# Kernel tuning notes

Hardware: AMD Instinct MI355X
Metric: run time of the kernel (lower is better)

## Reference

```python
import jax, jax.numpy as jnp
import numpy as np
from jax import lax

K = 16          # n_neighbors
EPS_BN = 1e-6   # torch BatchNorm2d eps in source


def _bn(x, g, be):
    # training-mode batch norm over (B, N, K) per channel, biased variance
    m = jnp.mean(x, axis=(0, 2, 3), keepdims=True)
    v = jnp.var(x, axis=(0, 2, 3), keepdims=True)
    return g[None, :, None, None] * (x - m) * lax.rsqrt(v + EPS_BN) + be[None, :, None, None]


def _smlp(x, W, b, g, be, act=None):
    # SharedMLP: 1x1 conv == channel matmul, then BN, then activation
    y = jnp.einsum('oc,bcnk->bonk', W, x) + b[None, :, None, None]
    y = _bn(y, g, be)
    return act(y) if act is not None else y


def _gather(f, nbrs):
    # f: (B, C, N), nbrs: (B, N, K) -> (B, C, N, K)
    return jax.vmap(lambda fb, nb: fb[:, nb])(f, nbrs)


def _attpool(x, Ws, W, b, g, be):
    # x: (B, C, N, K); scores: linear over C, softmax over K (dim=-2 after permute)
    s = jax.nn.softmax(jnp.einsum('oc,bcnk->bonk', Ws, x), axis=-1)
    pooled = jnp.sum(s * x, axis=-1, keepdims=True)  # (B, C, N, 1)
    return _smlp(pooled, W, b, g, be, jax.nn.relu)


def setup_inputs() -> dict:
    key = jax.random.key(0)
    ks = iter(jax.random.split(key, 40))
    B, N, n_in, n_out = 2, 8192, 64, 128
    C1 = n_out // 2

    def w(shape, s=0.05):
        return jax.random.normal(next(ks), shape, jnp.float32) * s

    inp = {
        'xyz': jax.random.normal(next(ks), (B, N, 3), jnp.float32),
        'feat_in': jax.random.normal(next(ks), (B, n_in, N, 1), jnp.float32),
        'm1_w': w((C1, n_in)), 'm1_b': jnp.zeros((C1,)), 'm1_g': jnp.ones((C1,)), 'm1_be': jnp.zeros((C1,)),
        'r1_w': w((C1, 10)), 'r1_b': jnp.zeros((C1,)), 'r1_g': jnp.ones((C1,)), 'r1_be': jnp.zeros((C1,)),
        'r2_w': w((C1, C1)), 'r2_b': jnp.zeros((C1,)), 'r2_g': jnp.ones((C1,)), 'r2_be': jnp.zeros((C1,)),
        'p1s_w': w((n_out, n_out)),
        'p1_w': w((C1, n_out)), 'p1_b': jnp.zeros((C1,)), 'p1_g': jnp.ones((C1,)), 'p1_be': jnp.zeros((C1,)),
        'p2s_w': w((n_out, n_out)),
        'p2_w': w((n_out, n_out)), 'p2_b': jnp.zeros((n_out,)), 'p2_g': jnp.ones((n_out,)), 'p2_be': jnp.zeros((n_out,)),
        'm2_w': w((2 * n_out, n_out)), 'm2_b': jnp.zeros((2 * n_out,)), 'm2_g': jnp.ones((2 * n_out,)), 'm2_be': jnp.zeros((2 * n_out,)),
        'sc_w': w((2 * n_out, n_in)), 'sc_b': jnp.zeros((2 * n_out,)), 'sc_g': jnp.ones((2 * n_out,)), 'sc_be': jnp.zeros((2 * n_out,)),
    }
    return inp


def reference(xyz, feat_in,
              m1_w, m1_b, m1_g, m1_be,
              r1_w, r1_b, r1_g, r1_be,
              r2_w, r2_b, r2_g, r2_be,
              p1s_w, p1_w, p1_b, p1_g, p1_be,
              p2s_w, p2_w, p2_b, p2_g, p2_be,
              m2_w, m2_b, m2_g, m2_be,
              sc_w, sc_b, sc_g, sc_be):
    # --- naive KNN (query == support) ---
    sq = jnp.sum(xyz * xyz, axis=-1)                       # (B, N)
    d2 = sq[:, :, None] + sq[:, None, :] - 2.0 * jnp.einsum('bnd,bmd->bnm', xyz, xyz)
    neg_d2, nbrs = lax.top_k(-d2, K)                       # (B, N, K)
    dist = jnp.sqrt(jnp.maximum(-neg_d2, 1e-12))

    # --- relative position encoding (10 channels) ---
    xyz_t = jnp.swapaxes(xyz, 1, 2)                        # (B, 3, N)
    nbr_xyz = _gather(xyz_t, nbrs)                         # (B, 3, N, K)
    ctr = jnp.broadcast_to(xyz_t[..., None], nbr_xyz.shape)
    rpe = jnp.concatenate([ctr, nbr_xyz, ctr - nbr_xyz, dist[:, None]], axis=1)  # (B,10,N,K)

    rpe1 = _smlp(rpe, r1_w, r1_b, r1_g, r1_be, jax.nn.relu)            # (B, C1, N, K)
    feats = _smlp(feat_in, m1_w, m1_b, m1_g, m1_be,
                  lambda x: jax.nn.leaky_relu(x, 0.2))                 # (B, C1, N, 1)

    # point feature augmentation 1 + attentive pool 1
    f = jnp.concatenate([rpe1, _gather(feats[:, :, :, 0], nbrs)], axis=1)  # (B, n_out, N, K)
    f = _attpool(f, p1s_w, p1_w, p1_b, p1_g, p1_be)                        # (B, C1, N, 1)

    # point feature augmentation 2 + attentive pool 2
    rpe2 = _smlp(rpe1, r2_w, r2_b, r2_g, r2_be, jax.nn.relu)
    f = jnp.concatenate([rpe2, _gather(f[:, :, :, 0], nbrs)], axis=1)      # (B, n_out, N, K)
    f = _attpool(f, p2s_w, p2_w, p2_b, p2_g, p2_be)                        # (B, n_out, N, 1)

    out = jax.nn.leaky_relu(
        _smlp(f, m2_w, m2_b, m2_g, m2_be) + _smlp(feat_in, sc_w, sc_b, sc_g, sc_be),
        0.01)                                                              # (B, 2*n_out, N, 1)
    return out
```

## Files before the change

### kernel.cpp

```cpp
#include <hip/hip_runtime.h>


#define NB 2
#define NPTS 8192
#define KNB 16

#define OFF_DIST 262144
#define OFF_YR1  524288
#define OFF_YM1  17301504
#define OFF_YP1  18350080
#define OFF_YP2  19398656
#define OFF_YM2  21495808
#define OFF_YSC  25690112
#define OFF_ST   29884416
#define WS_FLOATS 29886208

#define CAPC 22
#define OFF_PD   524288
#define OFF_TAU  4718592
#define OFF_CD   4734976
#define OFF_CI   10502144
#define OFF_CNT  16269312
#define OFF_PTS  17301504
#define OFF_POOL 21495808

#define INV_BNK 3.814697265625e-06f
#define INV_BN  6.103515625e-05f

typedef short bf16x8 __attribute__((ext_vector_type(8)));
typedef float f32x4 __attribute__((ext_vector_type(4)));

__device__ __forceinline__ float bf16f(unsigned short u) {
  return __uint_as_float(((unsigned)u) << 16);
}
__device__ __forceinline__ unsigned short fbf16(float f) {
  unsigned u = __float_as_uint(f);
  unsigned r = (u + 0x7fffu + ((u >> 16) & 1u)) >> 16;
  return (unsigned short)r;
}
__device__ __forceinline__ unsigned pack2(float a, float b) {
  return (unsigned)fbf16(a) | ((unsigned)fbf16(b) << 16);
}
__device__ __forceinline__ void mk_affine(const float* st, int C, int c, float invc,
                                          const float* g, const float* be,
                                          float& sc, float& sh) {
  float m = st[c] * invc;
  float v = fmaxf(st[C + c] * invc - m * m, 0.f);
  float inv = 1.0f / sqrtf(v + 1e-6f);
  sc = g[c] * inv;
  sh = be[c] - m * sc;
}

__device__ __forceinline__ float d2_of(float4 Q, float4 P) {
  return (Q.w + P.w) - 2.0f * fmaf(Q.x, P.x, fmaf(Q.y, P.y, Q.z * P.z));
}

__global__ __launch_bounds__(256) void knn_prep(const float* __restrict__ xyz,
                                                float4* __restrict__ pts) {
  int i = blockIdx.x * 256 + threadIdx.x;
  float x = xyz[i * 3 + 0], y = xyz[i * 3 + 1], z = xyz[i * 3 + 2];
  pts[i] = make_float4(x, y, z, x * x + y * y + z * z);
}

#define CHUNKS 16
#define CSZ 512
__global__ __launch_bounds__(256) void knn_part(const float4* __restrict__ pts,
                                                float* __restrict__ pd) {
  __shared__ float4 spt[CSZ];
  int tid = threadIdx.x;
  int c = blockIdx.x & 15;
  int qg = blockIdx.x >> 4;
  int b = qg >> 5;
  int gq = qg * 256 + tid;
  const float4* pb = pts + b * NPTS;
  for (int j = tid; j < CSZ; j += 256) spt[j] = pb[c * CSZ + j];
  __syncthreads();
  float4 Q = pts[gq];
  float bd[16];
#pragma unroll
  for (int t = 0; t < 16; ++t) bd[t] = 3.4e38f;
#define SE(a, bb) { float lo = fminf(e##a, e##bb); float hi = fmaxf(e##a, e##bb); e##a = lo; e##bb = hi; }
#define CB(i, j) { float lo = fminf(bd[i], bd[j]); float hi = fmaxf(bd[i], bd[j]); bd[i] = lo; bd[j] = hi; }
#pragma unroll 2
  for (int g = 0; g < CSZ / 8; ++g) {
    const float4* sp = &spt[g * 8];
    float e0 = d2_of(Q, sp[0]), e1 = d2_of(Q, sp[1]);
    float e2 = d2_of(Q, sp[2]), e3 = d2_of(Q, sp[3]);
    float e4 = d2_of(Q, sp[4]), e5 = d2_of(Q, sp[5]);
    float e6 = d2_of(Q, sp[6]), e7 = d2_of(Q, sp[7]);
    SE(0, 1) SE(2, 3) SE(4, 5) SE(6, 7)
    SE(0, 2) SE(1, 3) SE(4, 6) SE(5, 7)
    SE(1, 2) SE(5, 6)
    SE(0, 4) SE(1, 5) SE(2, 6) SE(3, 7)
    SE(2, 4) SE(3, 5)
    SE(1, 2) SE(3, 4) SE(5, 6)
    bd[8] = fminf(bd[8], e7);
    bd[9] = fminf(bd[9], e6);
    bd[10] = fminf(bd[10], e5);
    bd[11] = fminf(bd[11], e4);
    bd[12] = fminf(bd[12], e3);
    bd[13] = fminf(bd[13], e2);
    bd[14] = fminf(bd[14], e1);
    bd[15] = fminf(bd[15], e0);
    CB(0, 8) CB(1, 9) CB(2, 10) CB(3, 11) CB(4, 12) CB(5, 13) CB(6, 14) CB(7, 15)
    CB(0, 4) CB(1, 5) CB(2, 6) CB(3, 7) CB(8, 12) CB(9, 13) CB(10, 14) CB(11, 15)
    CB(0, 2) CB(1, 3) CB(4, 6) CB(5, 7) CB(8, 10) CB(9, 11) CB(12, 14) CB(13, 15)
    CB(0, 1) CB(2, 3) CB(4, 5) CB(6, 7) CB(8, 9) CB(10, 11) CB(12, 13) CB(14, 15)
  }
#undef SE
#undef CB
#pragma unroll
  for (int t = 0; t < 16; ++t) pd[(c * 16 + t) * 16384 + gq] = bd[t];
}

__global__ __launch_bounds__(256) void knn_tau(const float* __restrict__ pd,
                                               float* __restrict__ tau) {
  int tid = threadIdx.x;
  int l = tid & 63, w = tid >> 6;
  int sub = l >> 4, cl = l & 15;
  int gq = blockIdx.x * 16 + w * 4 + sub;
  int pos = 0;
  float hd = pd[(cl * 16) * 16384 + gq];
  for (int t = 0; t < 16; ++t) {
    float md = hd;
    int maux = cl;
#pragma unroll
    for (int m = 1; m < 16; m <<= 1) {
      float od = __shfl_xor(md, m, 64);
      int oa = __shfl_xor(maux, m, 64);
      bool take = (od < md) || (od == md && oa < maux);
      md = take ? od : md;
      maux = take ? oa : maux;
    }
    if (t == 15) {
      if (cl == 0) tau[gq] = md;
    } else {
      bool win = (hd == md) && (cl == maux);
      if (win) {
        pos++;
        hd = (pos < 16) ? pd[(cl * 16 + pos) * 16384 + gq] : 3.4e38f;
      }
    }
  }
}

__global__ __launch_bounds__(256) void knn_fcol(const float4* __restrict__ pts,
                                                const float* __restrict__ tau,
                                                float* __restrict__ cd,
                                                int* __restrict__ ci,
                                                int* __restrict__ cnts) {
  __shared__ float4 spt[CSZ];
  int tid = threadIdx.x;
  int c = blockIdx.x & 15;
  int qg = blockIdx.x >> 4;
  int b = qg >> 5;
  int gq = qg * 256 + tid;
  const float4* pb = pts + b * NPTS;
  for (int j = tid; j < CSZ; j += 256) spt[j] = pb[c * CSZ + j];
  __syncthreads();
  float4 Q = pts[gq];
  float tq = tau[gq];
  int cnt = 0;
  for (int jj = 0; jj < CSZ; ++jj) {
    float4 P = spt[jj];
    float d2 = d2_of(Q, P);
    if (d2 <= tq && cnt < CAPC) {
      cd[(size_t)(c * CAPC + cnt) * 16384 + gq] = d2;
      ci[(size_t)(c * CAPC + cnt) * 16384 + gq] = c * CSZ + jj;
      cnt++;
    }
  }
  cnts[c * 16384 + gq] = cnt;
}

__global__ __launch_bounds__(256) void knn_fin(const float* __restrict__ cd,
                                               const int* __restrict__ ci,
                                               const int* __restrict__ cnts,
                                               int* __restrict__ nbrs,
                                               float* __restrict__ dist) {
  __shared__ float sd[64][4][17];
  __shared__ int si[64][4][17];
  int tid = threadIdx.x;
  int ql = tid >> 2, sub = tid & 3;
  int gq = blockIdx.x * 64 + ql;
  float bd[16];
  int bi[16];
#pragma unroll
  for (int t = 0; t < 16; ++t) { bd[t] = 3.4e38f; bi[t] = 0x7fffffff; }
#pragma unroll
  for (int k = 0; k < 4; ++k) {
    int c = sub * 4 + k;
    int n = cnts[c * 16384 + gq];
    const float* cdq = cd + (size_t)c * CAPC * 16384 + gq;
    const int* ciq = ci + (size_t)c * CAPC * 16384 + gq;
    for (int s = 0; s < n; ++s) {
      float d = cdq[(size_t)s * 16384];
      int i = ciq[(size_t)s * 16384];
      bool ins = (d < bd[15]) || (d == bd[15] && i < bi[15]);
      bd[15] = ins ? d : bd[15];
      bi[15] = ins ? i : bi[15];
#pragma unroll
      for (int t = 15; t > 0; --t) {
        bool sw = (bd[t] < bd[t - 1]) || (bd[t] == bd[t - 1] && bi[t] < bi[t - 1]);
        float td = bd[t]; int ti = bi[t];
        bd[t] = sw ? bd[t - 1] : bd[t];
        bi[t] = sw ? bi[t - 1] : bi[t];
        bd[t - 1] = sw ? td : bd[t - 1];
        bi[t - 1] = sw ? ti : bi[t - 1];
      }
    }
  }
#pragma unroll
  for (int t = 0; t < 16; ++t) {
    sd[ql][sub][t] = bd[t];
    si[ql][sub][t] = bi[t];
  }
  sd[ql][sub][16] = 3.4e38f;
  si[ql][sub][16] = 0x7fffffff;
  __syncthreads();
  int p0 = 0, p1 = 0, p2 = 0, p3 = 0;
  for (int t = 0; t < 16; ++t) {
    float d0 = sd[ql][0][p0], d1 = sd[ql][1][p1];
    float d2 = sd[ql][2][p2], d3 = sd[ql][3][p3];
    int i0 = si[ql][0][p0], i1 = si[ql][1][p1];
    int i2 = si[ql][2][p2], i3 = si[ql][3][p3];
    float dm = d0; int im = i0; int sel = 0;
    if (d1 < dm || (d1 == dm && i1 < im)) { dm = d1; im = i1; sel = 1; }
    if (d2 < dm || (d2 == dm && i2 < im)) { dm = d2; im = i2; sel = 2; }
    if (d3 < dm || (d3 == dm && i3 < im)) { dm = d3; im = i3; sel = 3; }
    if (sel == 0) p0++; else if (sel == 1) p1++; else if (sel == 2) p2++; else p3++;
    if ((t >> 2) == sub) {
      dist[gq * 16 + t] = sqrtf(fmaxf(dm, 1e-12f));
      nbrs[gq * 16 + t] = im;
    }
  }
}

__global__ __launch_bounds__(256) void rpe_r1_kernel(
    const float* __restrict__ xyz, const int* __restrict__ nbrs,
    const float* __restrict__ dist, const float* __restrict__ W,
    const float* __restrict__ bias, float* __restrict__ yr1,
    float* __restrict__ st) {
  __shared__ float sW[64 * 11];
  __shared__ float sB[64];
  __shared__ float sP[4][64][9];
  int tid = threadIdx.x, lane = tid & 63, w = tid >> 6;
  for (int idx = tid; idx < 640; idx += 256) {
    int o = idx / 10, i = idx - o * 10;
    sW[o * 11 + i] = W[idx];
  }
  if (tid < 64) sB[tid] = bias[tid];
  __syncthreads();
  float wr[10];
#pragma unroll
  for (int i = 0; i < 10; ++i) wr[i] = sW[lane * 11 + i];
  float bs = sB[lane];
  float ps = 0.f, pq = 0.f;
  int base = (blockIdx.x * 4 + w) * 256;
  for (int bt = 0; bt < 4; ++bt) {
    int p = base + bt * 64 + lane;
    int b = p >> 17, rem = p & 131071, n = rem >> 4;
    const float* xb = xyz + b * NPTS * 3;
    int j = nbrs[p];
    float dd = dist[p];
    sP[w][lane][0] = xb[n * 3 + 0];
    sP[w][lane][1] = xb[n * 3 + 1];
    sP[w][lane][2] = xb[n * 3 + 2];
    sP[w][lane][3] = xb[j * 3 + 0];
    sP[w][lane][4] = xb[j * 3 + 1];
    sP[w][lane][5] = xb[j * 3 + 2];
    sP[w][lane][6] = dd;
    for (int t = 0; t < 64; ++t) {
      float cx = sP[w][t][0], cy = sP[w][t][1], cz = sP[w][t][2];
      float nx = sP[w][t][3], ny = sP[w][t][4], nz = sP[w][t][5];
      float dv = sP[w][t][6];
      float acc = bs;
      acc = fmaf(wr[0], cx, acc); acc = fmaf(wr[1], cy, acc); acc = fmaf(wr[2], cz, acc);
      acc = fmaf(wr[3], nx, acc); acc = fmaf(wr[4], ny, acc); acc = fmaf(wr[5], nz, acc);
      acc = fmaf(wr[6], cx - nx, acc); acc = fmaf(wr[7], cy - ny, acc); acc = fmaf(wr[8], cz - nz, acc);
      acc = fmaf(wr[9], dv, acc);
      yr1[(size_t)(base + bt * 64 + t) * 64 + lane] = acc;
      ps += acc; pq += acc * acc;
    }
  }
  unsafeAtomicAdd(&st[lane], ps);
  unsafeAtomicAdd(&st[64 + lane], pq);
}

__global__ __launch_bounds__(256) void m1_kernel(
    const float* __restrict__ feat, const float* __restrict__ W,
    const float* __restrict__ bias, float* __restrict__ ym1,
    float* __restrict__ st) {
  __shared__ float sW[64 * 64];
  int tid = threadIdx.x, lane = tid & 63, w = tid >> 6;
  for (int idx = tid; idx < 4096; idx += 256) {
    int o = idx >> 6, i = idx & 63;
    sW[i * 64 + o] = W[idx];
  }
  __syncthreads();
  float bs = bias[lane];
  float ps = 0.f, pq = 0.f;
  int base = (blockIdx.x * 4 + w) * 16;
  for (int it = 0; it < 4; ++it) {
    int p0 = base + it * 4;
    int b = p0 >> 13, n0 = p0 & 8191;
    const float* fb = feat + (size_t)b * 64 * NPTS + n0;
    float a0 = bs, a1 = bs, a2 = bs, a3 = bs;
#pragma unroll 4
    for (int i = 0; i < 64; ++i) {
      float wv = sW[i * 64 + lane];
      const float* fi = fb + (size_t)i * NPTS;
      a0 = fmaf(wv, fi[0], a0);
      a1 = fmaf(wv, fi[1], a1);
      a2 = fmaf(wv, fi[2], a2);
      a3 = fmaf(wv, fi[3], a3);
    }
    ym1[(size_t)p0 * 64 + lane] = a0;
    ym1[(size_t)(p0 + 1) * 64 + lane] = a1;
    ym1[(size_t)(p0 + 2) * 64 + lane] = a2;
    ym1[(size_t)(p0 + 3) * 64 + lane] = a3;
    ps += a0 + a1 + a2 + a3;
    pq += a0 * a0 + a1 * a1 + a2 * a2 + a3 * a3;
  }
  unsafeAtomicAdd(&st[lane], ps);
  unsafeAtomicAdd(&st[64 + lane], pq);
}

template <bool GLEAKY>
__global__ __launch_bounds__(256) void attpool_mfma(
    const float* __restrict__ ysrc, const float* __restrict__ ygat,
    const int* __restrict__ nbrs, const float* __restrict__ Wsc,
    const float* __restrict__ st_src, const float* __restrict__ g_src,
    const float* __restrict__ be_src, float inv_src,
    const float* __restrict__ st_gat, const float* __restrict__ g_gat,
    const float* __restrict__ be_gat, float inv_gat,
    float* __restrict__ pool) {
  __shared__ short sWsc[16384];
  __shared__ short sF[16384];
  int tid = threadIdx.x, l = tid & 63, w = tid >> 6;

#pragma unroll 4
  for (int it = 0; it < 32; ++it) {
    int e = it * 512 + tid * 2;
    int o = e >> 7, i = e & 127;
    unsigned v = pack2(Wsc[e], Wsc[e + 1]);
    *(unsigned*)((char*)sWsc + o * 256 + ((i * 2) ^ ((o & 7) << 4))) = v;
  }

  int cpair = tid & 31, c0 = cpair * 2, r8 = tid >> 5;
  float s0c, s0h, s1c, s1h, g0c, g0h, g1c, g1h;
  mk_affine(st_src, 64, c0, inv_src, g_src, be_src, s0c, s0h);
  mk_affine(st_src, 64, c0 + 1, inv_src, g_src, be_src, s1c, s1h);
  mk_affine(st_gat, 64, c0, inv_gat, g_gat, be_gat, g0c, g0h);
  mk_affine(st_gat, 64, c0 + 1, inv_gat, g_gat, be_gat, g1c, g1h);
  int prow_base = blockIdx.x * 128;
#pragma unroll 2
  for (int pass = 0; pass < 16; ++pass) {
    int row = pass * 8 + r8;
    int pr = prow_base + row;
    int sw = (row & 7) << 4;
    float2 sv = *(const float2*)&ysrc[(size_t)pr * 64 + c0];
    float v0 = fmaxf(fmaf(sv.x, s0c, s0h), 0.f);
    float v1 = fmaxf(fmaf(sv.y, s1c, s1h), 0.f);
    *(unsigned*)((char*)sF + row * 256 + ((c0 * 2) ^ sw)) = pack2(v0, v1);
    int b = pr >> 17;
    int j = nbrs[pr];
    float2 gv = *(const float2*)&ygat[(size_t)((b << 13) + j) * 64 + c0];
    float u0 = fmaf(gv.x, g0c, g0h);
    float u1 = fmaf(gv.y, g1c, g1h);
    u0 = GLEAKY ? (fminf(u0, 0.f) * 0.2f + fmaxf(u0, 0.f)) : fmaxf(u0, 0.f);
    u1 = GLEAKY ? (fminf(u1, 0.f) * 0.2f + fmaxf(u1, 0.f)) : fmaxf(u1, 0.f);
    *(unsigned*)((char*)sF + row * 256 + (((64 + c0) * 2) ^ sw)) = pack2(u0, u1);
  }
  __syncthreads();

  f32x4 acc[2][8];
#pragma unroll
  for (int m = 0; m < 2; ++m)
#pragma unroll
    for (int n = 0; n < 8; ++n) acc[m][n] = (f32x4){0.f, 0.f, 0.f, 0.f};
  int lsw = (l & 7) << 4;
#pragma unroll
  for (int kk = 0; kk < 4; ++kk) {
    int cs = (kk * 64 + ((l >> 4) << 4)) ^ lsw;
    bf16x8 a0 = *(const bf16x8*)((char*)sF + (w * 32 + (l & 15)) * 256 + cs);
    bf16x8 a1 = *(const bf16x8*)((char*)sF + (w * 32 + 16 + (l & 15)) * 256 + cs);
    bf16x8 bb[8];
#pragma unroll
    for (int n = 0; n < 8; ++n)
      bb[n] = *(const bf16x8*)((char*)sWsc + (n * 16 + (l & 15)) * 256 + cs);
#pragma unroll
    for (int n = 0; n < 8; ++n) {
      acc[0][n] = __builtin_amdgcn_mfma_f32_16x16x32_bf16(a0, bb[n], acc[0][n], 0, 0, 0);
      acc[1][n] = __builtin_amdgcn_mfma_f32_16x16x32_bf16(a1, bb[n], acc[1][n], 0, 0, 0);
    }
  }

#pragma unroll
  for (int m = 0; m < 2; ++m) {
    int p_glob = blockIdx.x * 8 + w * 2 + m;
    int rowbase = w * 32 + m * 16;
#pragma unroll
    for (int n = 0; n < 8; ++n) {
      f32x4 s = acc[m][n];
      float mx = fmaxf(fmaxf(s[0], s[1]), fmaxf(s[2], s[3]));
      mx = fmaxf(mx, __shfl_xor(mx, 16));
      mx = fmaxf(mx, __shfl_xor(mx, 32));
      float e0 = __expf(s[0] - mx), e1 = __expf(s[1] - mx);
      float e2 = __expf(s[2] - mx), e3 = __expf(s[3] - mx);
      float sm = (e0 + e1) + (e2 + e3);
      sm += __shfl_xor(sm, 16);
      sm += __shfl_xor(sm, 32);
      int cb2 = (n * 16 + (l & 15)) * 2;
      int k0 = (l >> 4) * 4;
      float num = 0.f;
      {
        int row = rowbase + k0;
        num = fmaf(e0, bf16f(*(const unsigned short*)((char*)sF + row * 256 + (cb2 ^ ((row & 7) << 4)))), num);
        row++;
        num = fmaf(e1, bf16f(*(const unsigned short*)((char*)sF + row * 256 + (cb2 ^ ((row & 7) << 4)))), num);
        row++;
        num = fmaf(e2, bf16f(*(const unsigned short*)((char*)sF + row * 256 + (cb2 ^ ((row & 7) << 4)))), num);
        row++;
        num = fmaf(e3, bf16f(*(const unsigned short*)((char*)sF + row * 256 + (cb2 ^ ((row & 7) << 4)))), num);
      }
      num += __shfl_xor(num, 16);
      num += __shfl_xor(num, 32);
      if ((l >> 4) == 0) pool[(size_t)p_glob * 128 + n * 16 + (l & 15)] = num / sm;
    }
  }
}

template <int COUT>
__global__ __launch_bounds__(256) void po_mfma(
    const float* __restrict__ pool, const float* __restrict__ W,
    const float* __restrict__ bias, float* __restrict__ yout,
    float* __restrict__ st_out) {
  __shared__ short sW2[COUT * 128];
  __shared__ short sF[64 * 128];
  __shared__ float sps[4][COUT];
  __shared__ float spq[4][COUT];
  int tid = threadIdx.x, l = tid & 63, w = tid >> 6;

#pragma unroll
  for (int it = 0; it < COUT / 4; ++it) {
    int e = it * 512 + tid * 2;
    int o = e >> 7, i = e & 127;
    *(unsigned*)((char*)sW2 + o * 256 + ((i * 2) ^ ((o & 7) << 4))) =
        pack2(W[e], W[e + 1]);
  }

  int c0 = (tid & 63) * 2, r4 = tid >> 6;
  size_t bp = (size_t)blockIdx.x * 64;
#pragma unroll 4
  for (int pass = 0; pass < 16; ++pass) {
    int row = pass * 4 + r4;
    float2 v = *(const float2*)&pool[(bp + row) * 128 + c0];
    *(unsigned*)((char*)sF + row * 256 + ((c0 * 2) ^ ((row & 7) << 4))) =
        pack2(v.x, v.y);
  }
  __syncthreads();

  f32x4 acc[COUT / 16];
#pragma unroll
  for (int n = 0; n < COUT / 16; ++n) acc[n] = (f32x4){0.f, 0.f, 0.f, 0.f};
  int lsw = (l & 7) << 4;
#pragma unroll
  for (int kk = 0; kk < 4; ++kk) {
    int cs = (kk * 64 + ((l >> 4) << 4)) ^ lsw;
    bf16x8 fa = *(const bf16x8*)((char*)sF + (w * 16 + (l & 15)) * 256 + cs);
#pragma unroll
    for (int n = 0; n < COUT / 16; ++n) {
      bf16x8 bb = *(const bf16x8*)((char*)sW2 + (n * 16 + (l & 15)) * 256 + cs);
      acc[n] = __builtin_amdgcn_mfma_f32_16x16x32_bf16(fa, bb, acc[n], 0, 0, 0);
    }
  }

#pragma unroll
  for (int n = 0; n < COUT / 16; ++n) {
    int o = n * 16 + (l & 15);
    float bo = bias[o];
    float ps = 0.f, pq = 0.f;
    int prow = w * 16 + (l >> 4) * 4;
#pragma unroll
    for (int r = 0; r < 4; ++r) {
      float v = acc[n][r] + bo;
      yout[(bp + prow + r) * COUT + o] = v;
      ps += v;
      pq += v * v;
    }
    ps += __shfl_xor(ps, 16); ps += __shfl_xor(ps, 32);
    pq += __shfl_xor(pq, 16); pq += __shfl_xor(pq, 32);
    if ((l >> 4) == 0) { sps[w][o] = ps; spq[w][o] = pq; }
  }
  __syncthreads();
  if (tid < COUT) {
    float s = sps[0][tid] + sps[1][tid] + sps[2][tid] + sps[3][tid];
    unsafeAtomicAdd(&st_out[tid], s);
  } else if (tid < 2 * COUT) {
    int c = tid - COUT;
    float s = spq[0][c] + spq[1][c] + spq[2][c] + spq[3][c];
    unsafeAtomicAdd(&st_out[COUT + c], s);
  }
}

__global__ __launch_bounds__(256) void r2_mfma(
    float* __restrict__ y, const float* __restrict__ W,
    const float* __restrict__ bias, const float* __restrict__ st_in,
    const float* __restrict__ g_in, const float* __restrict__ be_in,
    float* __restrict__ st_out) {
  __shared__ short sW2[4096];
  __shared__ short sF[8192];
  __shared__ float sps[4][64];
  __shared__ float spq[4][64];
  int tid = threadIdx.x, l = tid & 63, w = tid >> 6;

#pragma unroll
  for (int it = 0; it < 8; ++it) {
    int e = it * 512 + tid * 2;
    int o = e >> 6, i = e & 63;
    *(unsigned*)((char*)sW2 + o * 128 + ((i * 2) ^ ((o & 7) << 4))) =
        pack2(W[e], W[e + 1]);
  }

  int c0 = (tid & 31) * 2, r8 = tid >> 5;
  float a0c, a0h, a1c, a1h;
  mk_affine(st_in, 64, c0, INV_BNK, g_in, be_in, a0c, a0h);
  mk_affine(st_in, 64, c0 + 1, INV_BNK, g_in, be_in, a1c, a1h);
  size_t bp = (size_t)blockIdx.x * 128;
#pragma unroll 4
  for (int pass = 0; pass < 16; ++pass) {
    int row = pass * 8 + r8;
    float2 v = *(const float2*)&y[(bp + row) * 64 + c0];
    float v0 = fmaxf(fmaf(v.x, a0c, a0h), 0.f);
    float v1 = fmaxf(fmaf(v.y, a1c, a1h), 0.f);
    *(unsigned*)((char*)sF + row * 128 + ((c0 * 2) ^ ((row & 7) << 4))) =
        pack2(v0, v1);
  }
  __syncthreads();

  f32x4 acc[2][4];
#pragma unroll
  for (int m = 0; m < 2; ++m)
#pragma unroll
    for (int n = 0; n < 4; ++n) acc[m][n] = (f32x4){0.f, 0.f, 0.f, 0.f};
  int lsw = (l & 7) << 4;
#pragma unroll
  for (int kk = 0; kk < 2; ++kk) {
    int cs = (kk * 64 + ((l >> 4) << 4)) ^ lsw;
    bf16x8 fa0 = *(const bf16x8*)((char*)sF + (w * 32 + (l & 15)) * 128 + cs);
    bf16x8 fa1 = *(const bf16x8*)((char*)sF + (w * 32 + 16 + (l & 15)) * 128 + cs);
#pragma unroll
    for (int n = 0; n < 4; ++n) {
      bf16x8 bb = *(const bf16x8*)((char*)sW2 + (n * 16 + (l & 15)) * 128 + cs);
      acc[0][n] = __builtin_amdgcn_mfma_f32_16x16x32_bf16(fa0, bb, acc[0][n], 0, 0, 0);
      acc[1][n] = __builtin_amdgcn_mfma_f32_16x16x32_bf16(fa1, bb, acc[1][n], 0, 0, 0);
    }
  }

#pragma unroll
  for (int n = 0; n < 4; ++n) {
    int o = n * 16 + (l & 15);
    float bo = bias[o];
    float ps = 0.f, pq = 0.f;
#pragma unroll
    for (int m = 0; m < 2; ++m) {
      int prow = w * 32 + m * 16 + (l >> 4) * 4;
#pragma unroll
      for (int r = 0; r < 4; ++r) {
        float v = acc[m][n][r] + bo;
        y[(bp + prow + r) * 64 + o] = v;
        ps += v;
        pq += v * v;
      }
    }
    ps += __shfl_xor(ps, 16); ps += __shfl_xor(ps, 32);
    pq += __shfl_xor(pq, 16); pq += __shfl_xor(pq, 32);
    if ((l >> 4) == 0) { sps[w][o] = ps; spq[w][o] = pq; }
  }
  __syncthreads();
  if (tid < 64) {
    float s = sps[0][tid] + sps[1][tid] + sps[2][tid] + sps[3][tid];
    unsafeAtomicAdd(&st_out[tid], s);
  } else if (tid < 128) {
    int c = tid - 64;
    float s = spq[0][c] + spq[1][c] + spq[2][c] + spq[3][c];
    unsafeAtomicAdd(&st_out[64 + c], s);
  }
}

__global__ __launch_bounds__(256) void m2_mfma(
    const float* __restrict__ yp2, const float* __restrict__ W,
    const float* __restrict__ bias, const float* __restrict__ st_in,
    const float* __restrict__ g_in, const float* __restrict__ be_in,
    float* __restrict__ ym2, float* __restrict__ st_out) {
  __shared__ short sW2[128 * 128];
  __shared__ short sF[64 * 128];
  __shared__ float sps[4][128];
  __shared__ float spq[4][128];
  int tid = threadIdx.x, l = tid & 63, w = tid >> 6;
  int off = (blockIdx.x & 1) * 128;
  size_t bp = (size_t)(blockIdx.x >> 1) * 64;

  const float* Wh = W + (size_t)off * 128;
#pragma unroll
  for (int it = 0; it < 32; ++it) {
    int e = it * 512 + tid * 2;
    int o = e >> 7, i = e & 127;
    *(unsigned*)((char*)sW2 + o * 256 + ((i * 2) ^ ((o & 7) << 4))) =
        pack2(Wh[e], Wh[e + 1]);
  }

  int c0 = (tid & 63) * 2, r4 = tid >> 6;
  float a0c, a0h, a1c, a1h;
  mk_affine(st_in, 128, c0, INV_BN, g_in, be_in, a0c, a0h);
  mk_affine(st_in, 128, c0 + 1, INV_BN, g_in, be_in, a1c, a1h);
#pragma unroll 4
  for (int pass = 0; pass < 16; ++pass) {
    int row = pass * 4 + r4;
    float2 v = *(const float2*)&yp2[(bp + row) * 128 + c0];
    float v0 = fmaxf(fmaf(v.x, a0c, a0h), 0.f);
    float v1 = fmaxf(fmaf(v.y, a1c, a1h), 0.f);
    *(unsigned*)((char*)sF + row * 256 + ((c0 * 2) ^ ((row & 7) << 4))) =
        pack2(v0, v1);
  }
  __syncthreads();

  f32x4 acc[8];
#pragma unroll
  for (int n = 0; n < 8; ++n) acc[n] = (f32x4){0.f, 0.f, 0.f, 0.f};
  int lsw = (l & 7) << 4;
#pragma unroll
  for (int kk = 0; kk < 4; ++kk) {
    int cs = (kk * 64 + ((l >> 4) << 4)) ^ lsw;
    bf16x8 fa = *(const bf16x8*)((char*)sF + (w * 16 + (l & 15)) * 256 + cs);
#pragma unroll
    for (int n = 0; n < 8; ++n) {
      bf16x8 bb = *(const bf16x8*)((char*)sW2 + (n * 16 + (l & 15)) * 256 + cs);
      acc[n] = __builtin_amdgcn_mfma_f32_16x16x32_bf16(fa, bb, acc[n], 0, 0, 0);
    }
  }

#pragma unroll
  for (int n = 0; n < 8; ++n) {
    int o = n * 16 + (l & 15);
    float bo = bias[off + o];
    float ps = 0.f, pq = 0.f;
    int prow = w * 16 + (l >> 4) * 4;
#pragma unroll
    for (int r = 0; r < 4; ++r) {
      float v = acc[n][r] + bo;
      ym2[(bp + prow + r) * 256 + off + o] = v;
      ps += v;
      pq += v * v;
    }
    ps += __shfl_xor(ps, 16); ps += __shfl_xor(ps, 32);
    pq += __shfl_xor(pq, 16); pq += __shfl_xor(pq, 32);
    if ((l >> 4) == 0) { sps[w][o] = ps; spq[w][o] = pq; }
  }
  __syncthreads();
  if (tid < 128) {
    float s = sps[0][tid] + sps[1][tid] + sps[2][tid] + sps[3][tid];
    unsafeAtomicAdd(&st_out[off + tid], s);
  } else {
    int c = tid - 128;
    float s = spq[0][c] + spq[1][c] + spq[2][c] + spq[3][c];
    unsafeAtomicAdd(&st_out[256 + off + c], s);
  }
}

__global__ __launch_bounds__(256) void sc_kernel(
    const float* __restrict__ feat, const float* __restrict__ W,
    const float* __restrict__ bias, float* __restrict__ ysc,
    float* __restrict__ st_out) {
  __shared__ float sW[64 * 256];
  int tid = threadIdx.x, lane = tid & 63, w = tid >> 6;
  for (int idx = tid; idx < 16384; idx += 256) {
    int o = idx >> 6, i = idx & 63;
    sW[i * 256 + o] = W[idx];
  }
  __syncthreads();
  float bs0 = bias[lane], bs1 = bias[lane + 64], bs2 = bias[lane + 128], bs3 = bias[lane + 192];
  float ps0 = 0, ps1 = 0, ps2 = 0, ps3 = 0, pq0 = 0, pq1 = 0, pq2 = 0, pq3 = 0;
  int base = (blockIdx.x * 4 + w) * 16;
  for (int it = 0; it < 4; ++it) {
    int p0 = base + it * 4;
    int b = p0 >> 13, n0 = p0 & 8191;
    const float* fb = feat + (size_t)b * 64 * NPTS + n0;
    float acc[4][4];
#pragma unroll
    for (int j = 0; j < 4; ++j) {
      acc[j][0] = bs0; acc[j][1] = bs1; acc[j][2] = bs2; acc[j][3] = bs3;
    }
#pragma unroll 2
    for (int i = 0; i < 64; ++i) {
      float w0 = sW[i * 256 + lane], w1 = sW[i * 256 + 64 + lane];
      float w2 = sW[i * 256 + 128 + lane], w3 = sW[i * 256 + 192 + lane];
      const float* fi = fb + (size_t)i * NPTS;
#pragma unroll
      for (int j = 0; j < 4; ++j) {
        float fv = fi[j];
        acc[j][0] = fmaf(w0, fv, acc[j][0]);
        acc[j][1] = fmaf(w1, fv, acc[j][1]);
        acc[j][2] = fmaf(w2, fv, acc[j][2]);
        acc[j][3] = fmaf(w3, fv, acc[j][3]);
      }
    }
#pragma unroll
    for (int j = 0; j < 4; ++j) {
      size_t ob = (size_t)(p0 + j) * 256;
      ysc[ob + lane] = acc[j][0];
      ysc[ob + 64 + lane] = acc[j][1];
      ysc[ob + 128 + lane] = acc[j][2];
      ysc[ob + 192 + lane] = acc[j][3];
      ps0 += acc[j][0]; pq0 += acc[j][0] * acc[j][0];
      ps1 += acc[j][1]; pq1 += acc[j][1] * acc[j][1];
      ps2 += acc[j][2]; pq2 += acc[j][2] * acc[j][2];
      ps3 += acc[j][3]; pq3 += acc[j][3] * acc[j][3];
    }
  }
  unsafeAtomicAdd(&st_out[lane], ps0); unsafeAtomicAdd(&st_out[256 + lane], pq0);
  unsafeAtomicAdd(&st_out[64 + lane], ps1); unsafeAtomicAdd(&st_out[256 + 64 + lane], pq1);
  unsafeAtomicAdd(&st_out[128 + lane], ps2); unsafeAtomicAdd(&st_out[256 + 128 + lane], pq2);
  unsafeAtomicAdd(&st_out[192 + lane], ps3); unsafeAtomicAdd(&st_out[256 + 192 + lane], pq3);
}

__global__ __launch_bounds__(256) void combine_kernel(
    const float* __restrict__ ym2, const float* __restrict__ ysc,
    const float* __restrict__ st_m2, const float* __restrict__ g_m2,
    const float* __restrict__ be_m2, const float* __restrict__ st_sc,
    const float* __restrict__ g_sc, const float* __restrict__ be_sc,
    float* __restrict__ out) {
  __shared__ float tile[64][65];
  int tid = threadIdx.x;
  int bid = blockIdx.x;
  int b = bid >> 9;
  int rem = bid & 511;
  int ct = rem >> 7;
  int nt = rem & 127;
  int cbase = ct * 64, n0 = nt * 64;
  int cl = tid & 63;
  int ch = cbase + cl;
  float sm2, hm2, ssc2, hsc2;
  mk_affine(st_m2, 256, ch, INV_BN, g_m2, be_m2, sm2, hm2);
  mk_affine(st_sc, 256, ch, INV_BN, g_sc, be_sc, ssc2, hsc2);
  int rr = tid >> 6;
  for (int it = 0; it < 16; ++it) {
    int n = n0 + rr + it * 4;
    size_t o = (size_t)((b << 13) + n) * 256 + ch;
    float v = fmaf(ym2[o], sm2, hm2) + fmaf(ysc[o], ssc2, hsc2);
    v = fminf(v, 0.f) * 0.01f + fmaxf(v, 0.f);
    tile[rr + it * 4][cl] = v;
  }
  __syncthreads();
  int nl = tid & 63, cc = tid >> 6;
  for (int it = 0; it < 16; ++it) {
    int c = cc + it * 4;
    out[(size_t)(b * 256 + cbase + c) * NPTS + n0 + nl] = tile[nl][c];
  }
}

extern "C" void kernel_launch(void* const* d_in, const int* in_sizes, int n_in,
                              void* d_out, int out_size, void* d_ws,
                              size_t ws_size, hipStream_t stream) {
  const float* xyz = (const float*)d_in[0];
  const float* feat = (const float*)d_in[1];
  const float* m1_w = (const float*)d_in[2];
  const float* m1_b = (const float*)d_in[3];
  const float* m1_g = (const float*)d_in[4];
  const float* m1_be = (const float*)d_in[5];
  const float* r1_w = (const float*)d_in[6];
  const float* r1_b = (const float*)d_in[7];
  const float* r1_g = (const float*)d_in[8];
  const float* r1_be = (const float*)d_in[9];
  const float* r2_w = (const float*)d_in[10];
  const float* r2_b = (const float*)d_in[11];
  const float* r2_g = (const float*)d_in[12];
  const float* r2_be = (const float*)d_in[13];
  const float* p1s_w = (const float*)d_in[14];
  const float* p1_w = (const float*)d_in[15];
  const float* p1_b = (const float*)d_in[16];
  const float* p1_g = (const float*)d_in[17];
  const float* p1_be = (const float*)d_in[18];
  const float* p2s_w = (const float*)d_in[19];
  const float* p2_w = (const float*)d_in[20];
  const float* p2_b = (const float*)d_in[21];
  const float* p2_g = (const float*)d_in[22];
  const float* p2_be = (const float*)d_in[23];
  const float* m2_w = (const float*)d_in[24];
  const float* m2_b = (const float*)d_in[25];
  const float* m2_g = (const float*)d_in[26];
  const float* m2_be = (const float*)d_in[27];
  const float* sc_w = (const float*)d_in[28];
  const float* sc_b = (const float*)d_in[29];
  const float* sc_g = (const float*)d_in[30];
  const float* sc_be = (const float*)d_in[31];

  if (ws_size < (size_t)WS_FLOATS * sizeof(float)) return;

  float* ws = (float*)d_ws;
  int* nbrs = (int*)ws;
  float* dist = ws + OFF_DIST;
  float* yr1 = ws + OFF_YR1;
  float* ym1 = ws + OFF_YM1;
  float* yp1 = ws + OFF_YP1;
  float* yp2 = ws + OFF_YP2;
  float* ym2 = ws + OFF_YM2;
  float* ysc = ws + OFF_YSC;
  float* st = ws + OFF_ST;
  float* st_r1 = st;
  float* st_m1 = st + 128;
  float* st_p1 = st + 256;
  float* st_r2 = st + 384;
  float* st_p2 = st + 512;
  float* st_m2 = st + 768;
  float* st_sc = st + 1280;
  float* pd = ws + OFF_PD;
  float* tau = ws + OFF_TAU;
  float* cd = ws + OFF_CD;
  int* ci = (int*)(ws + OFF_CI);
  int* cnts = (int*)(ws + OFF_CNT);
  float4* pts4 = (float4*)(ws + OFF_PTS);
  float* pool = ws + OFF_POOL;

  hipMemsetAsync(st, 0, 1792 * sizeof(float), stream);
  knn_prep<<<64, 256, 0, stream>>>(xyz, pts4);
  knn_part<<<NB * 32 * CHUNKS, 256, 0, stream>>>(pts4, pd);
  knn_tau<<<1024, 256, 0, stream>>>(pd, tau);
  knn_fcol<<<NB * 32 * CHUNKS, 256, 0, stream>>>(pts4, tau, cd, ci, cnts);
  knn_fin<<<256, 256, 0, stream>>>(cd, ci, cnts, nbrs, dist);
  rpe_r1_kernel<<<256, 256, 0, stream>>>(xyz, nbrs, dist, r1_w, r1_b, yr1, st_r1);
  m1_kernel<<<256, 256, 0, stream>>>(feat, m1_w, m1_b, ym1, st_m1);
  attpool_mfma<true><<<2048, 256, 0, stream>>>(
      yr1, ym1, nbrs, p1s_w,
      st_r1, r1_g, r1_be, INV_BNK,
      st_m1, m1_g, m1_be, INV_BN, pool);
  po_mfma<64><<<256, 256, 0, stream>>>(pool, p1_w, p1_b, yp1, st_p1);
  r2_mfma<<<2048, 256, 0, stream>>>(yr1, r2_w, r2_b, st_r1, r1_g, r1_be, st_r2);
  attpool_mfma<false><<<2048, 256, 0, stream>>>(
      yr1, yp1, nbrs, p2s_w,
      st_r2, r2_g, r2_be, INV_BNK,
      st_p1, p1_g, p1_be, INV_BN, pool);
  po_mfma<128><<<256, 256, 0, stream>>>(pool, p2_w, p2_b, yp2, st_p2);
  m2_mfma<<<512, 256, 0, stream>>>(yp2, m2_w, m2_b, st_p2, p2_g, p2_be, ym2, st_m2);
  sc_kernel<<<256, 256, 0, stream>>>(feat, sc_w, sc_b, ysc, st_sc);
  combine_kernel<<<1024, 256, 0, stream>>>(ym2, ysc, st_m2, m2_g, m2_be,
                                           st_sc, sc_g, sc_be, (float*)d_out);
}
```

Before: 522.4 us.

## Estimate KNN threshold from a point subset instead of an exact partial top-k

Drops the exact per-chunk top-16 pass and its merge kernel. A new kernel computes, for each query, the 16th-smallest distance among the first 1024 points of its batch. Four lanes share a query and merge their sorted lists with shuffles, and the result is used as the candidate threshold. That threshold is a valid upper bound but looser than the exact value, so the per-chunk candidate capacity grows from 22 to 28 and the workspace offsets are rearranged. The distance work before the collection pass drops sharply, at the cost of more candidates per chunk and a risk of overflowing the capacity on unlucky inputs.

```diff
diff --git a/kernel.cpp b/kernel.cpp
--- a/kernel.cpp
+++ b/kernel.cpp
@@ -15,12 +15,11 @@
 #define OFF_ST   29884416
 #define WS_FLOATS 29886208
 
-#define CAPC 22
-#define OFF_PD   524288
-#define OFF_TAU  4718592
-#define OFF_CD   4734976
-#define OFF_CI   10502144
-#define OFF_CNT  16269312
+#define CAPC 28
+#define OFF_TAU  524288
+#define OFF_CD   540672
+#define OFF_CI   7880704
+#define OFF_CNT  15220736
 #define OFF_PTS  17301504
 #define OFF_POOL 21495808
 
@@ -62,88 +61,59 @@
   pts[i] = make_float4(x, y, z, x * x + y * y + z * z);
 }
 
+#define SAMP 1024
+__global__ __launch_bounds__(256) void knn_samp(const float4* __restrict__ pts,
+                                                float* __restrict__ tau) {
+  __shared__ float4 spt[SAMP];
+  int tid = threadIdx.x;
+  int b = blockIdx.x >> 7;
+  int gq = blockIdx.x * 64 + (tid >> 2);
+  int sub = tid & 3;
+  const float4* pb = pts + b * NPTS;
+  for (int j = tid; j < SAMP; j += 256) spt[j] = pb[j];
+  __syncthreads();
+  float4 Q = pts[gq];
+  float bd[16];
+#pragma unroll
+  for (int t = 0; t < 16; ++t) bd[t] = 3.4e38f;
+  int j0 = sub * 256;
+#pragma unroll 4
+  for (int jj = 0; jj < 256; ++jj) {
+    float4 P = spt[j0 + jj];
+    float d2 = d2_of(Q, P);
+    bd[15] = fminf(bd[15], d2);
+#pragma unroll
+    for (int t = 15; t > 0; --t) {
+      float lo = fminf(bd[t - 1], bd[t]);
+      float hi = fmaxf(bd[t - 1], bd[t]);
+      bd[t - 1] = lo;
+      bd[t] = hi;
+    }
+  }
+  float c[16];
+#pragma unroll
+  for (int i = 0; i < 16; ++i) {
+    float ob = __shfl_xor(bd[15 - i], 1, 64);
+    c[i] = fminf(bd[i], ob);
+  }
+#define CE(i, j) { float lo = fminf(c[i], c[j]); float hi = fmaxf(c[i], c[j]); c[i] = lo; c[j] = hi; }
+  CE(0, 8) CE(1, 9) CE(2, 10) CE(3, 11) CE(4, 12) CE(5, 13) CE(6, 14) CE(7, 15)
+  CE(0, 4) CE(1, 5) CE(2, 6) CE(3, 7) CE(8, 12) CE(9, 13) CE(10, 14) CE(11, 15)
+  CE(0, 2) CE(1, 3) CE(4, 6) CE(5, 7) CE(8, 10) CE(9, 11) CE(12, 14) CE(13, 15)
+  CE(0, 1) CE(2, 3) CE(4, 5) CE(6, 7) CE(8, 9) CE(10, 11) CE(12, 13) CE(14, 15)
+#undef CE
+  float m = 0.f;
+#pragma unroll
+  for (int i = 0; i < 16; ++i) {
+    float od = __shfl_xor(c[15 - i], 2, 64);
+    float v = fminf(c[i], od);
+    m = (i == 0) ? v : fmaxf(m, v);
+  }
+  if (sub == 0) tau[gq] = m;
+}
+
 #define CHUNKS 16
 #define CSZ 512
-__global__ __launch_bounds__(256) void knn_part(const float4* __restrict__ pts,
-                                                float* __restrict__ pd) {
-  __shared__ float4 spt[CSZ];
-  int tid = threadIdx.x;
-  int c = blockIdx.x & 15;
-  int qg = blockIdx.x >> 4;
-  int b = qg >> 5;
-  int gq = qg * 256 + tid;
-  const float4* pb = pts + b * NPTS;
-  for (int j = tid; j < CSZ; j += 256) spt[j] = pb[c * CSZ + j];
-  __syncthreads();
-  float4 Q = pts[gq];
-  float bd[16];
-#pragma unroll
-  for (int t = 0; t < 16; ++t) bd[t] = 3.4e38f;
-#define SE(a, bb) { float lo = fminf(e##a, e##bb); float hi = fmaxf(e##a, e##bb); e##a = lo; e##bb = hi; }
-#define CB(i, j) { float lo = fminf(bd[i], bd[j]); float hi = fmaxf(bd[i], bd[j]); bd[i] = lo; bd[j] = hi; }
-#pragma unroll 2
-  for (int g = 0; g < CSZ / 8; ++g) {
-    const float4* sp = &spt[g * 8];
-    float e0 = d2_of(Q, sp[0]), e1 = d2_of(Q, sp[1]);
-    float e2 = d2_of(Q, sp[2]), e3 = d2_of(Q, sp[3]);
-    float e4 = d2_of(Q, sp[4]), e5 = d2_of(Q, sp[5]);
-    float e6 = d2_of(Q, sp[6]), e7 = d2_of(Q, sp[7]);
-    SE(0, 1) SE(2, 3) SE(4, 5) SE(6, 7)
-    SE(0, 2) SE(1, 3) SE(4, 6) SE(5, 7)
-    SE(1, 2) SE(5, 6)
-    SE(0, 4) SE(1, 5) SE(2, 6) SE(3, 7)
-    SE(2, 4) SE(3, 5)
-    SE(1, 2) SE(3, 4) SE(5, 6)
-    bd[8] = fminf(bd[8], e7);
-    bd[9] = fminf(bd[9], e6);
-    bd[10] = fminf(bd[10], e5);
-    bd[11] = fminf(bd[11], e4);
-    bd[12] = fminf(bd[12], e3);
-    bd[13] = fminf(bd[13], e2);
-    bd[14] = fminf(bd[14], e1);
-    bd[15] = fminf(bd[15], e0);
-    CB(0, 8) CB(1, 9) CB(2, 10) CB(3, 11) CB(4, 12) CB(5, 13) CB(6, 14) CB(7, 15)
-    CB(0, 4) CB(1, 5) CB(2, 6) CB(3, 7) CB(8, 12) CB(9, 13) CB(10, 14) CB(11, 15)
-    CB(0, 2) CB(1, 3) CB(4, 6) CB(5, 7) CB(8, 10) CB(9, 11) CB(12, 14) CB(13, 15)
-    CB(0, 1) CB(2, 3) CB(4, 5) CB(6, 7) CB(8, 9) CB(10, 11) CB(12, 13) CB(14, 15)
-  }
-#undef SE
-#undef CB
-#pragma unroll
-  for (int t = 0; t < 16; ++t) pd[(c * 16 + t) * 16384 + gq] = bd[t];
-}
-
-__global__ __launch_bounds__(256) void knn_tau(const float* __restrict__ pd,
-                                               float* __restrict__ tau) {
-  int tid = threadIdx.x;
-  int l = tid & 63, w = tid >> 6;
-  int sub = l >> 4, cl = l & 15;
-  int gq = blockIdx.x * 16 + w * 4 + sub;
-  int pos = 0;
-  float hd = pd[(cl * 16) * 16384 + gq];
-  for (int t = 0; t < 16; ++t) {
-    float md = hd;
-    int maux = cl;
-#pragma unroll
-    for (int m = 1; m < 16; m <<= 1) {
-      float od = __shfl_xor(md, m, 64);
-      int oa = __shfl_xor(maux, m, 64);
-      bool take = (od < md) || (od == md && oa < maux);
-      md = take ? od : md;
-      maux = take ? oa : maux;
-    }
-    if (t == 15) {
-      if (cl == 0) tau[gq] = md;
-    } else {
-      bool win = (hd == md) && (cl == maux);
-      if (win) {
-        pos++;
-        hd = (pos < 16) ? pd[(cl * 16 + pos) * 16384 + gq] : 3.4e38f;
-      }
-    }
-  }
-}
-
 __global__ __launch_bounds__(256) void knn_fcol(const float4* __restrict__ pts,
                                                 const float* __restrict__ tau,
                                                 float* __restrict__ cd,
@@ -815,7 +785,6 @@
   float* st_p2 = st + 512;
   float* st_m2 = st + 768;
   float* st_sc = st + 1280;
-  float* pd = ws + OFF_PD;
   float* tau = ws + OFF_TAU;
   float* cd = ws + OFF_CD;
   int* ci = (int*)(ws + OFF_CI);
@@ -825,8 +794,7 @@
 
   hipMemsetAsync(st, 0, 1792 * sizeof(float), stream);
   knn_prep<<<64, 256, 0, stream>>>(xyz, pts4);
-  knn_part<<<NB * 32 * CHUNKS, 256, 0, stream>>>(pts4, pd);
-  knn_tau<<<1024, 256, 0, stream>>>(pd, tau);
+  knn_samp<<<256, 256, 0, stream>>>(pts4, tau);
   knn_fcol<<<NB * 32 * CHUNKS, 256, 0, stream>>>(pts4, tau, cd, ci, cnts);
   knn_fin<<<256, 256, 0, stream>>>(cd, ci, cnts, nbrs, dist);
   rpe_r1_kernel<<<256, 256, 0, stream>>>(xyz, nbrs, dist, r1_w, r1_b, yr1, st_r1);
```

Result: slower. 567.7 us (+8.7%).
